# Kernel tuning notes

Hardware: AMD Instinct MI355X
Metric: run time of the kernel (lower is better)

The kernel has to match this reference:

```python
import jax, jax.numpy as jnp
import numpy as np


def setup_inputs() -> dict:
    key = jax.random.key(0)
    k1, k2, k3, k4 = jax.random.split(key, 4)
    B, S, D, R = 32, 512, 1024, 256
    batch = jax.random.normal(k1, (B, S, D), dtype=jnp.float32)
    # params initialized uniform(-0.05, 0.05) in the original
    proj_L = jax.random.uniform(k2, (D, R), minval=-0.05, maxval=0.05, dtype=jnp.float32)
    proj_R = jax.random.uniform(k3, (R, D), minval=-0.05, maxval=0.05, dtype=jnp.float32)
    bias = jax.random.uniform(k4, (1,), minval=-0.05, maxval=0.05, dtype=jnp.float32)
    return {"batch": batch, "proj_L": proj_L, "proj_R": proj_R, "bias": bias}


def reference(batch, proj_L, proj_R, bias):
    # logits[b,i,j] = batch[b,i] @ (L @ R) @ batch[b,j] + bias
    # Computed as (batch @ L) @ (batch @ R^T)^T -- two batched GEMMs,
    # avoiding the O(B*S^2*D) expanded intermediate of the original.
    # Dropout is identity in eval mode.
    left = jnp.einsum('bsd,dr->bsr', batch, proj_L)   # [B,S,R]
    right = jnp.einsum('rd,btd->brt', proj_R, batch)  # [B,R,S]
    logits = jnp.einsum('bsr,brt->bst', left, right) + bias[0]
    return logits
```

## Files before the change

### kernel.cpp

```cpp
#include <hip/hip_runtime.h>
#include <hip/hip_bf16.h>
#include <stdint.h>

typedef __attribute__((ext_vector_type(8))) __bf16 bf16x8;
typedef __attribute__((ext_vector_type(4))) float f32x4;

static constexpr int Bb = 32, Ss = 512, Dd = 1024, Rr = 256;
static constexpr int M1 = Bb * Ss;

__device__ __forceinline__ void gload_lds16(const void* g, void* l) {
  __builtin_amdgcn_global_load_lds(
      (const __attribute__((address_space(1))) void*)g,
      (__attribute__((address_space(3))) void*)l, 16, 0, 0);
}

__global__ __launch_bounds__(256) void prep_kernel(
    const float* __restrict__ L, const float* __restrict__ R,
    __bf16* __restrict__ Lt, __bf16* __restrict__ Rb) {
  int i = blockIdx.x * 256 + threadIdx.x;
  if (i < Rr * Dd) {
    int r = i >> 10;
    int d = i & (Dd - 1);
    Lt[i] = (__bf16)L[d * Rr + r];
    Rb[i] = (__bf16)R[i];
  }
}

__global__ __launch_bounds__(256, 2) void proj_gemm(
    const float* __restrict__ batch,
    const __bf16* __restrict__ BtL,
    const __bf16* __restrict__ BtR,
    __bf16* __restrict__ outL,
    __bf16* __restrict__ outR) {
  const int nt = blockIdx.x;
  const int mt = blockIdx.y;
  const int which = blockIdx.z;
  const __bf16* Bt = which ? BtR : BtL;
  __bf16* out = which ? outR : outL;
  const int m0 = mt * 128, n0 = nt * 128;

  __shared__ __align__(16) char smem[16384];
  char* At = smem;
  char* Btile = smem + 8192;

  const int t = threadIdx.x;
  const int lane = t & 63;
  const int wave = t >> 6;
  const int wr = wave >> 1, wc = wave & 1;

  f32x4 acc[4][4] = {};

  for (int k0 = 0; k0 < Dd; k0 += 32) {
    __syncthreads();
#pragma unroll
    for (int p = 0; p < 2; ++p) {
      int e = p * 256 + t;
      int row = e >> 2;
      int kk = (e & 3) * 8;
      const float* src = batch + (size_t)(m0 + row) * Dd + k0 + kk;
      f32x4 f0 = *(const f32x4*)src;
      f32x4 f1 = *(const f32x4*)(src + 4);
      bf16x8 v;
      v[0] = (__bf16)f0[0]; v[1] = (__bf16)f0[1];
      v[2] = (__bf16)f0[2]; v[3] = (__bf16)f0[3];
      v[4] = (__bf16)f1[0]; v[5] = (__bf16)f1[1];
      v[6] = (__bf16)f1[2]; v[7] = (__bf16)f1[3];
      *(bf16x8*)(At + e * 16) = v;
    }
#pragma unroll
    for (int p = 0; p < 2; ++p) {
      int e = p * 256 + t;
      int row = e >> 2;
      int kp = e & 3;
      gload_lds16(Bt + (size_t)(n0 + row) * Dd + k0 + kp * 8, Btile + e * 16);
    }
    __syncthreads();

    bf16x8 a[4], b[4];
#pragma unroll
    for (int m = 0; m < 4; ++m)
      a[m] = *(const bf16x8*)(At + (wr * 64 + m * 16 + (lane & 15)) * 64 +
                              (lane >> 4) * 16);
#pragma unroll
    for (int n = 0; n < 4; ++n)
      b[n] = *(const bf16x8*)(Btile + (wc * 64 + n * 16 + (lane & 15)) * 64 +
                              (lane >> 4) * 16);
#pragma unroll
    for (int m = 0; m < 4; ++m)
#pragma unroll
      for (int n = 0; n < 4; ++n)
        acc[m][n] =
            __builtin_amdgcn_mfma_f32_16x16x32_bf16(a[m], b[n], acc[m][n], 0, 0, 0);
  }

  const int col = lane & 15, rgrp = lane >> 4;
#pragma unroll
  for (int m = 0; m < 4; ++m) {
    int r0 = m0 + wr * 64 + m * 16 + rgrp * 4;
#pragma unroll
    for (int n = 0; n < 4; ++n) {
      int c = n0 + wc * 64 + n * 16 + col;
#pragma unroll
      for (int i = 0; i < 4; ++i)
        out[(size_t)(r0 + i) * Rr + c] = (__bf16)acc[m][n][i];
    }
  }
}

__global__ __launch_bounds__(256, 2) void score_gemm(
    const __bf16* __restrict__ left,
    const __bf16* __restrict__ right,
    const float* __restrict__ biasp,
    float* __restrict__ out) {
  const int nt = blockIdx.x;
  const int mt = blockIdx.y;
  const int bz = blockIdx.z;
  const __bf16* A = left + (size_t)bz * Ss * Rr;
  const __bf16* Bt = right + (size_t)bz * Ss * Rr;
  float* O = out + (size_t)bz * Ss * Ss;
  const int m0 = mt * 128, n0 = nt * 128;

  __shared__ __align__(16) char smem[16384];
  char* At = smem;
  char* Btile = smem + 8192;

  const int t = threadIdx.x;
  const int lane = t & 63;
  const int wave = t >> 6;
  const int wr = wave >> 1, wc = wave & 1;

  f32x4 acc[4][4] = {};

  for (int k0 = 0; k0 < Rr; k0 += 32) {
    __syncthreads();
#pragma unroll
    for (int p = 0; p < 2; ++p) {
      int e = p * 256 + t;
      int row = e >> 2;
      int kp = e & 3;
      gload_lds16(A + (size_t)(m0 + row) * Rr + k0 + kp * 8, At + e * 16);
      gload_lds16(Bt + (size_t)(n0 + row) * Rr + k0 + kp * 8, Btile + e * 16);
    }
    __syncthreads();

    bf16x8 a[4], b[4];
#pragma unroll
    for (int m = 0; m < 4; ++m)
      a[m] = *(const bf16x8*)(At + (wr * 64 + m * 16 + (lane & 15)) * 64 +
                              (lane >> 4) * 16);
#pragma unroll
    for (int n = 0; n < 4; ++n)
      b[n] = *(const bf16x8*)(Btile + (wc * 64 + n * 16 + (lane & 15)) * 64 +
                              (lane >> 4) * 16);
#pragma unroll
    for (int m = 0; m < 4; ++m)
#pragma unroll
      for (int n = 0; n < 4; ++n)
        acc[m][n] =
            __builtin_amdgcn_mfma_f32_16x16x32_bf16(a[m], b[n], acc[m][n], 0, 0, 0);
  }

  const float bias = *biasp;
  const int col = lane & 15, rgrp = lane >> 4;
#pragma unroll
  for (int m = 0; m < 4; ++m) {
    int r0 = m0 + wr * 64 + m * 16 + rgrp * 4;
#pragma unroll
    for (int n = 0; n < 4; ++n) {
      int c = n0 + wc * 64 + n * 16 + col;
#pragma unroll
      for (int i = 0; i < 4; ++i)
        O[(size_t)(r0 + i) * Ss + c] = acc[m][n][i] + bias;
    }
  }
}

extern "C" void kernel_launch(void* const* d_in, const int* in_sizes, int n_in,
                              void* d_out, int out_size, void* d_ws,
                              size_t ws_size, hipStream_t stream) {
  const float* batch = (const float*)d_in[0];
  const float* projL = (const float*)d_in[1];
  const float* projR = (const float*)d_in[2];
  const float* bias = (const float*)d_in[3];
  float* out = (float*)d_out;

  char* ws = (char*)d_ws;
  __bf16* left = (__bf16*)(ws);
  __bf16* right = (__bf16*)(ws + 8388608);
  __bf16* Lt = (__bf16*)(ws + 16777216);
  __bf16* Rb = (__bf16*)(ws + 16777216 + 524288);

  prep_kernel<<<dim3(1024), dim3(256), 0, stream>>>(projL, projR, Lt, Rb);
  proj_gemm<<<dim3(2, 128, 2), dim3(256), 0, stream>>>(batch, Lt, Rb, left,
                                                       right);
  score_gemm<<<dim3(4, 4, 32), dim3(256), 0, stream>>>(left, right, bias, out);
}
```

Baseline: 58.60 us.

## Double-buffer LDS with K=64 tiles, XOR swizzle, and concatenated L/R weights

Both GEMMs now use double-buffered LDS tiles with K=64 per stage and prefetch the next stage while computing the current one. The batch fp32 loads go into registers before compute and are converted and written to LDS afterward. An XOR swizzle on the 16-byte groups is meant to remove LDS bank conflicts. The L and R projection weights are concatenated into one 512-wide B matrix, so each proj_gemm block reads batch once per N-tile in a single grid rather than separate z-slices. LDS use grows to 64KB per block, which with launch_bounds(256,2) may limit occupancy.

```diff
diff --git a/kernel.cpp b/kernel.cpp
--- a/kernel.cpp
+++ b/kernel.cpp
@@ -5,7 +5,7 @@
 typedef __attribute__((ext_vector_type(8))) __bf16 bf16x8;
 typedef __attribute__((ext_vector_type(4))) float f32x4;
 
-static constexpr int Bb = 32, Ss = 512, Dd = 1024, Rr = 256;
+static constexpr int Bb = 32, Ss = 512, Dd = 1024, Rr = 256, Nn = 512;
 static constexpr int M1 = Bb * Ss;
 
 __device__ __forceinline__ void gload_lds16(const void* g, void* l) {
@@ -16,32 +16,24 @@
 
 __global__ __launch_bounds__(256) void prep_kernel(
     const float* __restrict__ L, const float* __restrict__ R,
-    __bf16* __restrict__ Lt, __bf16* __restrict__ Rb) {
+    __bf16* __restrict__ Bt) {
   int i = blockIdx.x * 256 + threadIdx.x;
-  if (i < Rr * Dd) {
-    int r = i >> 10;
-    int d = i & (Dd - 1);
-    Lt[i] = (__bf16)L[d * Rr + r];
-    Rb[i] = (__bf16)R[i];
-  }
+  int n = i >> 10;
+  int d = i & (Dd - 1);
+  float v = (n < Rr) ? L[d * Rr + n] : R[(size_t)(n - Rr) * Dd + d];
+  Bt[i] = (__bf16)v;
 }
 
 __global__ __launch_bounds__(256, 2) void proj_gemm(
     const float* __restrict__ batch,
-    const __bf16* __restrict__ BtL,
-    const __bf16* __restrict__ BtR,
+    const __bf16* __restrict__ Bt,
     __bf16* __restrict__ outL,
     __bf16* __restrict__ outR) {
   const int nt = blockIdx.x;
   const int mt = blockIdx.y;
-  const int which = blockIdx.z;
-  const __bf16* Bt = which ? BtR : BtL;
-  __bf16* out = which ? outR : outL;
   const int m0 = mt * 128, n0 = nt * 128;
 
-  __shared__ __align__(16) char smem[16384];
-  char* At = smem;
-  char* Btile = smem + 8192;
+  __shared__ __align__(16) char smem[65536];
 
   const int t = threadIdx.x;
   const int lane = t & 63;
@@ -49,57 +41,99 @@
   const int wr = wave >> 1, wc = wave & 1;
 
   f32x4 acc[4][4] = {};
-
-  for (int k0 = 0; k0 < Dd; k0 += 32) {
-    __syncthreads();
-#pragma unroll
-    for (int p = 0; p < 2; ++p) {
-      int e = p * 256 + t;
-      int row = e >> 2;
-      int kk = (e & 3) * 8;
-      const float* src = batch + (size_t)(m0 + row) * Dd + k0 + kk;
-      f32x4 f0 = *(const f32x4*)src;
-      f32x4 f1 = *(const f32x4*)(src + 4);
+  f32x4 areg[8];
+
+  auto issueA = [&](int k0) {
+#pragma unroll
+    for (int q = 0; q < 4; ++q) {
+      int e = q * 256 + t;
+      int row = e >> 3, g = e & 7;
+      const float* src = batch + (size_t)(m0 + row) * Dd + k0 + g * 8;
+      areg[2 * q] = *(const f32x4*)src;
+      areg[2 * q + 1] = *(const f32x4*)(src + 4);
+    }
+  };
+  auto writeA = [&](int buf) {
+    char* Ab = smem + buf * 16384;
+#pragma unroll
+    for (int q = 0; q < 4; ++q) {
+      int e = q * 256 + t;
+      int row = e >> 3, g = e & 7;
+      int gs = g ^ (row & 7);
       bf16x8 v;
+      f32x4 f0 = areg[2 * q], f1 = areg[2 * q + 1];
       v[0] = (__bf16)f0[0]; v[1] = (__bf16)f0[1];
       v[2] = (__bf16)f0[2]; v[3] = (__bf16)f0[3];
       v[4] = (__bf16)f1[0]; v[5] = (__bf16)f1[1];
       v[6] = (__bf16)f1[2]; v[7] = (__bf16)f1[3];
-      *(bf16x8*)(At + e * 16) = v;
-    }
-#pragma unroll
-    for (int p = 0; p < 2; ++p) {
+      *(bf16x8*)(Ab + (row * 8 + gs) * 16) = v;
+    }
+  };
+  auto stageB = [&](int buf, int k0) {
+    char* Bbuf = smem + 32768 + buf * 16384;
+#pragma unroll
+    for (int p = 0; p < 4; ++p) {
       int e = p * 256 + t;
-      int row = e >> 2;
-      int kp = e & 3;
-      gload_lds16(Bt + (size_t)(n0 + row) * Dd + k0 + kp * 8, Btile + e * 16);
-    }
+      int row = e >> 3, g = e & 7;
+      int gs = g ^ (row & 7);
+      gload_lds16(Bt + (size_t)(n0 + row) * Dd + k0 + gs * 8,
+                  Bbuf + e * 16);
+    }
+  };
+  auto compute = [&](int buf) {
+    char* Ab = smem + buf * 16384;
+    char* Bbuf = smem + 32768 + buf * 16384;
+#pragma unroll
+    for (int kk = 0; kk < 2; ++kk) {
+      bf16x8 a[4], b[4];
+#pragma unroll
+      for (int m = 0; m < 4; ++m) {
+        int row = wr * 64 + m * 16 + (lane & 15);
+        int g = kk * 4 + (lane >> 4);
+        a[m] = *(const bf16x8*)(Ab + (row * 8 + (g ^ (row & 7))) * 16);
+      }
+#pragma unroll
+      for (int n = 0; n < 4; ++n) {
+        int row = wc * 64 + n * 16 + (lane & 15);
+        int g = kk * 4 + (lane >> 4);
+        b[n] = *(const bf16x8*)(Bbuf + (row * 8 + (g ^ (row & 7))) * 16);
+      }
+#pragma unroll
+      for (int m = 0; m < 4; ++m)
+#pragma unroll
+        for (int n = 0; n < 4; ++n)
+          acc[m][n] = __builtin_amdgcn_mfma_f32_16x16x32_bf16(a[m], b[n],
+                                                              acc[m][n], 0, 0, 0);
+    }
+  };
+
+  issueA(0);
+  stageB(0, 0);
+  writeA(0);
+  __syncthreads();
+
+  int cur = 0;
+  for (int it = 0; it < 16; ++it) {
+    int nxt = cur ^ 1;
+    if (it < 15) {
+      issueA((it + 1) * 64);
+      stageB(nxt, (it + 1) * 64);
+    }
+    compute(cur);
+    if (it < 15) writeA(nxt);
     __syncthreads();
-
-    bf16x8 a[4], b[4];
-#pragma unroll
-    for (int m = 0; m < 4; ++m)
-      a[m] = *(const bf16x8*)(At + (wr * 64 + m * 16 + (lane & 15)) * 64 +
-                              (lane >> 4) * 16);
-#pragma unroll
-    for (int n = 0; n < 4; ++n)
-      b[n] = *(const bf16x8*)(Btile + (wc * 64 + n * 16 + (lane & 15)) * 64 +
-                              (lane >> 4) * 16);
-#pragma unroll
-    for (int m = 0; m < 4; ++m)
-#pragma unroll
-      for (int n = 0; n < 4; ++n)
-        acc[m][n] =
-            __builtin_amdgcn_mfma_f32_16x16x32_bf16(a[m], b[n], acc[m][n], 0, 0, 0);
-  }
-
+    cur = nxt;
+  }
+
+  __bf16* out = (n0 < Rr) ? outL : outR;
+  const int cb = n0 & (Rr - 1);
   const int col = lane & 15, rgrp = lane >> 4;
 #pragma unroll
   for (int m = 0; m < 4; ++m) {
     int r0 = m0 + wr * 64 + m * 16 + rgrp * 4;
 #pragma unroll
     for (int n = 0; n < 4; ++n) {
-      int c = n0 + wc * 64 + n * 16 + col;
+      int c = cb + wc * 64 + n * 16 + col;
 #pragma unroll
       for (int i = 0; i < 4; ++i)
         out[(size_t)(r0 + i) * Rr + c] = (__bf16)acc[m][n][i];
@@ -116,13 +150,11 @@
   const int mt = blockIdx.y;
   const int bz = blockIdx.z;
   const __bf16* A = left + (size_t)bz * Ss * Rr;
-  const __bf16* Bt = right + (size_t)bz * Ss * Rr;
+  const __bf16* B = right + (size_t)bz * Ss * Rr;
   float* O = out + (size_t)bz * Ss * Ss;
   const int m0 = mt * 128, n0 = nt * 128;
 
-  __shared__ __align__(16) char smem[16384];
-  char* At = smem;
-  char* Btile = smem + 8192;
+  __shared__ __align__(16) char smem[65536];
 
   const int t = threadIdx.x;
   const int lane = t & 63;
@@ -131,33 +163,54 @@
 
   f32x4 acc[4][4] = {};
 
-  for (int k0 = 0; k0 < Rr; k0 += 32) {
+  auto stage = [&](int buf, int k0) {
+    char* Ab = smem + buf * 16384;
+    char* Bbuf = smem + 32768 + buf * 16384;
+#pragma unroll
+    for (int p = 0; p < 4; ++p) {
+      int e = p * 256 + t;
+      int row = e >> 3, g = e & 7;
+      int gs = g ^ (row & 7);
+      gload_lds16(A + (size_t)(m0 + row) * Rr + k0 + gs * 8, Ab + e * 16);
+      gload_lds16(B + (size_t)(n0 + row) * Rr + k0 + gs * 8, Bbuf + e * 16);
+    }
+  };
+  auto compute = [&](int buf) {
+    char* Ab = smem + buf * 16384;
+    char* Bbuf = smem + 32768 + buf * 16384;
+#pragma unroll
+    for (int kk = 0; kk < 2; ++kk) {
+      bf16x8 a[4], b[4];
+#pragma unroll
+      for (int m = 0; m < 4; ++m) {
+        int row = wr * 64 + m * 16 + (lane & 15);
+        int g = kk * 4 + (lane >> 4);
+        a[m] = *(const bf16x8*)(Ab + (row * 8 + (g ^ (row & 7))) * 16);
+      }
+#pragma unroll
+      for (int n = 0; n < 4; ++n) {
+        int row = wc * 64 + n * 16 + (lane & 15);
+        int g = kk * 4 + (lane >> 4);
+        b[n] = *(const bf16x8*)(Bbuf + (row * 8 + (g ^ (row & 7))) * 16);
+      }
+#pragma unroll
+      for (int m = 0; m < 4; ++m)
+#pragma unroll
+        for (int n = 0; n < 4; ++n)
+          acc[m][n] = __builtin_amdgcn_mfma_f32_16x16x32_bf16(a[m], b[n],
+                                                              acc[m][n], 0, 0, 0);
+    }
+  };
+
+  stage(0, 0);
+  __syncthreads();
+  int cur = 0;
+  for (int it = 0; it < 4; ++it) {
+    int nxt = cur ^ 1;
+    if (it < 3) stage(nxt, (it + 1) * 64);
+    compute(cur);
     __syncthreads();
-#pragma unroll
-    for (int p = 0; p < 2; ++p) {
-      int e = p * 256 + t;
-      int row = e >> 2;
-      int kp = e & 3;
-      gload_lds16(A + (size_t)(m0 + row) * Rr + k0 + kp * 8, At + e * 16);
-      gload_lds16(Bt + (size_t)(n0 + row) * Rr + k0 + kp * 8, Btile + e * 16);
-    }
-    __syncthreads();
-
-    bf16x8 a[4], b[4];
-#pragma unroll
-    for (int m = 0; m < 4; ++m)
-      a[m] = *(const bf16x8*)(At + (wr * 64 + m * 16 + (lane & 15)) * 64 +
-                              (lane >> 4) * 16);
-#pragma unroll
-    for (int n = 0; n < 4; ++n)
-      b[n] = *(const bf16x8*)(Btile + (wc * 64 + n * 16 + (lane & 15)) * 64 +
-                              (lane >> 4) * 16);
-#pragma unroll
-    for (int m = 0; m < 4; ++m)
-#pragma unroll
-      for (int n = 0; n < 4; ++n)
-        acc[m][n] =
-            __builtin_amdgcn_mfma_f32_16x16x32_bf16(a[m], b[n], acc[m][n], 0, 0, 0);
+    cur = nxt;
   }
 
   const float bias = *biasp;
@@ -187,11 +240,9 @@
   char* ws = (char*)d_ws;
   __bf16* left = (__bf16*)(ws);
   __bf16* right = (__bf16*)(ws + 8388608);
-  __bf16* Lt = (__bf16*)(ws + 16777216);
-  __bf16* Rb = (__bf16*)(ws + 16777216 + 524288);
-
-  prep_kernel<<<dim3(1024), dim3(256), 0, stream>>>(projL, projR, Lt, Rb);
-  proj_gemm<<<dim3(2, 128, 2), dim3(256), 0, stream>>>(batch, Lt, Rb, left,
-                                                       right);
+  __bf16* Btc = (__bf16*)(ws + 16777216);
+
+  prep_kernel<<<dim3(2048), dim3(256), 0, stream>>>(projL, projR, Btc);
+  proj_gemm<<<dim3(4, 128), dim3(256), 0, stream>>>(batch, Btc, left, right);
   score_gemm<<<dim3(4, 4, 32), dim3(256), 0, stream>>>(left, right, bias, out);
 }
```

Result: slower. 66.35 us (+13.2%).
